# Performance work log

Measured on AMD Instinct MI355X. Metric: run time of the kernel, lower is better.

## Reference

```python
import jax, jax.numpy as jnp
import numpy as np

B, S, D, C, K, V = 128, 512, 300, 300, 3, 30000  # batch, seq, embed=hidden, capsule, categories, vocab
PAD_INDEX = 0
SQUASH_EPS = 1e-8
MASK_NEG = -1e9


def squash(x, axis=-1):
    # v * (|v|^2 / (1+|v|^2)) / |v|
    sq = jnp.sum(x * x, axis=axis, keepdims=True)
    return (sq / (1.0 + sq)) * x / jnp.sqrt(sq + SQUASH_EPS)


def setup_inputs() -> dict:
    key = jax.random.key(0)
    ks = jax.random.split(key, 11)
    return {
        "sentence": jax.random.randint(ks[0], (B, S), 0, V),
        "aspect": jax.random.randint(ks[1], (B,), 0, V),
        "category_alpha": jax.random.uniform(ks[2], (B, S), dtype=jnp.float32),
        "embed": jax.random.normal(ks[3], (V, D), dtype=jnp.float32) * 0.02,
        "W_s": jax.random.normal(ks[4], (D, C), dtype=jnp.float32) * 0.02,
        "b_s": jnp.zeros((C,), dtype=jnp.float32),
        "W_a": jax.random.normal(ks[5], (D, C), dtype=jnp.float32) * 0.02,
        "b_a": jnp.zeros((C,), dtype=jnp.float32),
        "W_att": jax.random.normal(ks[6], (C, C), dtype=jnp.float32) * 0.02,
        "guide_capsule": jax.random.normal(ks[7], (K, C), dtype=jnp.float32) * 0.02,
        "guide_weight": jax.random.normal(ks[8], (C, C), dtype=jnp.float32) * 0.02,
        "scale": jnp.asarray(5.0, dtype=jnp.float32),
    }


def reference(sentence, aspect, category_alpha, embed, W_s, b_s, W_a, b_a,
              W_att, guide_capsule, guide_weight, scale):
    mask = sentence != PAD_INDEX                      # [B,S]
    emb = embed[sentence]                             # [B,S,D]
    asp = embed[aspect]                               # [B,D]

    # element_wise_mul (vectorized): per-token alpha weighting
    caml = emb * category_alpha[..., None]            # [B,S,D]
    cavl = jnp.sum(caml, axis=1)                      # [B,D] (unused in non-Cav path)
    del cavl

    # _sentence_encode stand-in (abstract in source): alpha-weighted embeddings
    sent_enc = caml                                   # [B,S,hidden=D]

    primary = squash(sent_enc @ W_s + b_s)            # [B,S,C]
    aspect_capsule = squash(asp @ W_a + b_a)          # [B,C]

    # bilinear attention weights with padding mask, softmax over sequence
    scores = jnp.einsum('bsc,cd,bd->bs', primary, W_att, aspect_capsule)
    scores = jnp.where(mask, scores, MASK_NEG)
    norm_weight = jax.nn.softmax(scores, axis=-1)     # [B,S]

    # capsule-guided routing
    guide = squash(guide_capsule)                     # [K,C]
    gm = jnp.einsum('bsc,cd,kd->bsk', primary, guide_weight, guide)
    gm = jax.nn.softmax(gm, axis=-1) * norm_weight[..., None] * scale
    category_capsule = squash(jnp.einsum('bsk,bsc->bkc', gm, primary))  # [B,K,C]

    return jnp.sqrt(jnp.sum(category_capsule * category_capsule, axis=-1))  # [B,K]
```

## Files before the change

kernel.cpp:

```cpp
#include <hip/hip_runtime.h>

#define NV 30000
#define NB 128
#define NS 512
#define ND 300
#define NC 300
#define CP 304
#define KPAD 320
#define MASK_NEG -1e9f
#define SQ_EPS 1e-8f

typedef __attribute__((ext_vector_type(4))) float f32x4;
typedef __attribute__((ext_vector_type(8))) __bf16 bf16x8;

__device__ __forceinline__ unsigned short f2bf(float x){
  unsigned int u = __float_as_uint(x);
  u += 0x7FFFu + ((u >> 16) & 1u);
  return (unsigned short)(u >> 16);
}
__device__ __forceinline__ float bf2f(unsigned short h){
  return __uint_as_float(((unsigned int)h) << 16);
}

__global__ __launch_bounds__(320) void k0_prep(
    const float* __restrict__ Ws, const float* __restrict__ Watt,
    const float* __restrict__ Gw, const float* __restrict__ bs,
    const float* __restrict__ gcap,
    unsigned short* __restrict__ wt, float* __restrict__ att_t,
    float* __restrict__ gwt, float* __restrict__ bsp, float* __restrict__ gpad)
{
  int bid = blockIdx.x, tid = threadIdx.x;
  __shared__ float red[320];
  if (bid < 80) {
    #pragma unroll
    for (int r = 0; r < 4; r++){
      int id = bid*1280 + r*320 + tid;
      int n = id / 320, k = id - n*320;
      float v = (n < NC && k < ND) ? Ws[k*NC + n] : 0.f;
      wt[n*KPAD + k] = f2bf(v);
    }
  } else if (bid < 151) {
    #pragma unroll
    for (int r = 0; r < 4; r++){
      int id = (bid-80)*1280 + r*320 + tid;
      if (id < ND*NC){ int c = id / ND, d = id - c*ND; att_t[d*CP + c] = Watt[id]; }
    }
  } else if (bid < 222) {
    #pragma unroll
    for (int r = 0; r < 4; r++){
      int id = (bid-151)*1280 + r*320 + tid;
      if (id < ND*NC){ int c = id / ND, d = id - c*ND; gwt[d*CP + c] = Gw[id]; }
    }
  } else if (bid == 222) {
    if (tid < CP) bsp[tid] = (tid < NC) ? bs[tid] : 0.f;
  } else {
    int k = bid - 223;
    float g = (tid < NC) ? gcap[k*NC + tid] : 0.f;
    red[tid] = g*g; __syncthreads();
    if (tid < 64){
      float s = red[tid]+red[tid+64]+red[tid+128]+red[tid+192]+red[tid+256];
      #pragma unroll
      for (int off = 32; off > 0; off >>= 1) s += __shfl_xor(s, off);
      if (tid == 0) red[0] = s;
    }
    __syncthreads();
    float sq = red[0];
    float ss = (sq/(1.f+sq))/sqrtf(sq + SQ_EPS);
    if (tid < CP) gpad[k*CP + tid] = g*ss;
  }
}

#define ANB 4
__global__ __launch_bounds__(320) void k2_aspect(
    const int* __restrict__ aspect, const float* __restrict__ embed,
    const float* __restrict__ Wa, const float* __restrict__ ba,
    const float* __restrict__ att_t, const float* __restrict__ gwt,
    const float* __restrict__ gpad,
    float* __restrict__ tbuf, float* __restrict__ gbuf)
{
  int bid = blockIdx.x, tid = threadIdx.x;
  __shared__ float red[320];
  if (bid < NB/ANB) {
    __shared__ float vec[ANB][CP];
    int b0 = bid*ANB;
    for (int i = tid; i < ANB*CP; i += 320){
      int bi = i / CP, c = i - bi*CP;
      int a = aspect[b0 + bi];
      vec[bi][c] = (c < ND) ? embed[(size_t)a*ND + c] : 0.f;
    }
    __syncthreads();
    float z[ANB] = {0.f,0.f,0.f,0.f};
    if (tid < NC){
      #pragma unroll
      for (int i = 0; i < ANB; i++) z[i] = ba[tid];
      for (int d = 0; d < ND; d++){
        float wv = Wa[d*NC + tid];
        #pragma unroll
        for (int i = 0; i < ANB; i++) z[i] += vec[i][d]*wv;
      }
    }
    float ssv[ANB];
    for (int i = 0; i < ANB; i++){
      red[tid] = (tid < NC) ? z[i]*z[i] : 0.f;
      __syncthreads();
      if (tid < 64){
        float s = red[tid]+red[tid+64]+red[tid+128]+red[tid+192]+red[tid+256];
        #pragma unroll
        for (int off = 32; off > 0; off >>= 1) s += __shfl_xor(s, off);
        if (tid == 0) red[0] = s;
      }
      __syncthreads();
      float sq = red[0];
      ssv[i] = (sq/(1.f+sq))/sqrtf(sq + SQ_EPS);
      __syncthreads();
    }
    if (tid < CP){
      #pragma unroll
      for (int i = 0; i < ANB; i++) vec[i][tid] = (tid < NC) ? z[i]*ssv[i] : 0.f;
    }
    __syncthreads();
    float t[ANB] = {0.f,0.f,0.f,0.f};
    if (tid < NC){
      for (int d = 0; d < ND; d++){
        float av = att_t[d*CP + tid];
        #pragma unroll
        for (int i = 0; i < ANB; i++) t[i] += av*vec[i][d];
      }
    }
    if (tid < CP){
      #pragma unroll
      for (int i = 0; i < ANB; i++) tbuf[(b0+i)*CP + tid] = (tid < NC) ? t[i] : 0.f;
    }
  } else {
    int k = bid - NB/ANB;
    float t = 0.f;
    if (tid < NC){
      for (int d = 0; d < ND; d++) t += gwt[d*CP + tid]*gpad[k*CP + d];
    }
    if (tid < CP) gbuf[k*CP + tid] = (tid < NC) ? t : 0.f;
  }
}

#define BM 128
#define BKT 64
#define LDK 72
__global__ __launch_bounds__(512) void k1_gemm(
    const float* __restrict__ embed, const unsigned short* __restrict__ wt,
    unsigned short* __restrict__ E)
{
  __shared__ unsigned short lds_a[BM*LDK];
  __shared__ unsigned short lds_b[320*LDK];
  int tid = threadIdx.x;
  int lane = tid & 63, wid = tid >> 6;
  int wrow = wid >> 2, wcol = wid & 3;
  int rowbase = blockIdx.x * BM;
  f32x4 acc[4][5];
  f32x4 zero = {0.f,0.f,0.f,0.f};
  #pragma unroll
  for (int m = 0; m < 4; m++)
    #pragma unroll
    for (int n = 0; n < 5; n++) acc[m][n] = zero;

  for (int k0 = 0; k0 < KPAD; k0 += BKT){
    #pragma unroll
    for (int r = 0; r < 4; r++){
      int id = r*512 + tid;
      int row = id >> 4, k4 = (id & 15) << 2;
      int gk = k0 + k4, grow = rowbase + row;
      float4 v = {0.f,0.f,0.f,0.f};
      if (grow < NV && gk < ND) v = *(const float4*)(embed + (size_t)grow*ND + gk);
      unsigned int lo = (unsigned int)f2bf(v.x) | ((unsigned int)f2bf(v.y) << 16);
      unsigned int hi = (unsigned int)f2bf(v.z) | ((unsigned int)f2bf(v.w) << 16);
      uint2 pk; pk.x = lo; pk.y = hi;
      *(uint2*)(lds_a + row*LDK + k4) = pk;
    }
    #pragma unroll
    for (int r = 0; r < 5; r++){
      int id = r*512 + tid;
      int n = id >> 3, koff = (id & 7) << 3;
      uint4 v = *(const uint4*)(wt + n*KPAD + k0 + koff);
      *(uint4*)(lds_b + n*LDK + koff) = v;
    }
    __syncthreads();
    #pragma unroll
    for (int kk = 0; kk < BKT; kk += 32){
      bf16x8 af[4], bfr[5];
      int kidx = kk + (lane >> 4)*8;
      int arow = wrow*64 + (lane & 15);
      int brow = wcol*80 + (lane & 15);
      #pragma unroll
      for (int m = 0; m < 4; m++) af[m] = *(const bf16x8*)(lds_a + (arow + m*16)*LDK + kidx);
      #pragma unroll
      for (int n = 0; n < 5; n++) bfr[n] = *(const bf16x8*)(lds_b + (brow + n*16)*LDK + kidx);
      #pragma unroll
      for (int m = 0; m < 4; m++)
        #pragma unroll
        for (int n = 0; n < 5; n++)
          acc[m][n] = __builtin_amdgcn_mfma_f32_16x16x32_bf16(af[m], bfr[n], acc[m][n], 0, 0, 0);
    }
    __syncthreads();
  }
  int colb = wcol*80 + (lane & 15);
  int rowb = rowbase + wrow*64 + ((lane >> 4) << 2);
  #pragma unroll
  for (int m = 0; m < 4; m++)
    #pragma unroll
    for (int n = 0; n < 5; n++)
      #pragma unroll
      for (int j = 0; j < 4; j++){
        int row = rowb + m*16 + j;
        int col = colb + n*16;
        if (row < NV && col < CP) E[(size_t)row*CP + col] = f2bf(acc[m][n][j]);
      }
}

__global__ __launch_bounds__(256) void k3_token(
    const int* __restrict__ sentence, const float* __restrict__ alphaA,
    const unsigned short* __restrict__ E, const float* __restrict__ tbuf,
    const float* __restrict__ gbuf, const float* __restrict__ bsp,
    float* __restrict__ scoreB, float* __restrict__ ssB, float* __restrict__ uuB)
{
  int tid = threadIdx.x;
  int lane = tid & 63;
  int wg = (blockIdx.x << 2) + (tid >> 6);
  int tok = sentence[wg];
  float al = alphaA[wg];
  int b = wg >> 9;
  const unsigned short* erow = E + (size_t)tok*CP;
  const float* trow = tbuf + b*CP;
  float sq = 0.f, sc = 0.f, u0 = 0.f, u1 = 0.f, u2 = 0.f;
  auto body = [&](int c){
    uint2 e2 = *(const uint2*)(erow + c);
    float4 tv = *(const float4*)(trow + c);
    float4 g0 = *(const float4*)(gbuf + c);
    float4 g1 = *(const float4*)(gbuf + CP + c);
    float4 g2 = *(const float4*)(gbuf + 2*CP + c);
    float4 bv = *(const float4*)(bsp + c);
    float y0 = al*bf2f((unsigned short)(e2.x & 0xffffu)) + bv.x;
    float y1 = al*bf2f((unsigned short)(e2.x >> 16)) + bv.y;
    float y2 = al*bf2f((unsigned short)(e2.y & 0xffffu)) + bv.z;
    float y3 = al*bf2f((unsigned short)(e2.y >> 16)) + bv.w;
    sq += y0*y0 + y1*y1 + y2*y2 + y3*y3;
    sc += y0*tv.x + y1*tv.y + y2*tv.z + y3*tv.w;
    u0 += y0*g0.x + y1*g0.y + y2*g0.z + y3*g0.w;
    u1 += y0*g1.x + y1*g1.y + y2*g1.z + y3*g1.w;
    u2 += y0*g2.x + y1*g2.y + y2*g2.z + y3*g2.w;
  };
  body(lane << 2);
  if (lane < 12) body(256 + (lane << 2));
  #pragma unroll
  for (int off = 32; off > 0; off >>= 1){
    sq += __shfl_xor(sq, off);
    sc += __shfl_xor(sc, off);
    u0 += __shfl_xor(u0, off);
    u1 += __shfl_xor(u1, off);
    u2 += __shfl_xor(u2, off);
  }
  if (lane == 0){
    float ssv = (sq/(1.f+sq))/sqrtf(sq + SQ_EPS);
    scoreB[wg] = (tok != 0) ? ssv*sc : MASK_NEG;
    ssB[wg] = ssv;
    uuB[wg*3+0] = ssv*u0;
    uuB[wg*3+1] = ssv*u1;
    uuB[wg*3+2] = ssv*u2;
  }
}

__global__ __launch_bounds__(512) void k4_softmax(
    const float* __restrict__ scoreB, const float* __restrict__ uuB,
    const float* __restrict__ ssB, const float* __restrict__ alphaA,
    const float* __restrict__ scale_p,
    float* __restrict__ coef, float* __restrict__ sb)
{
  int b = blockIdx.x, tid = threadIdx.x;
  int idx = (b << 9) + tid;
  __shared__ float red[512];
  float scv = scoreB[idx];
  red[tid] = scv; __syncthreads();
  if (tid < 64){
    float s = red[tid];
    #pragma unroll
    for (int o = 64; o < 512; o += 64) s = fmaxf(s, red[tid+o]);
    #pragma unroll
    for (int off = 32; off > 0; off >>= 1) s = fmaxf(s, __shfl_xor(s, off));
    if (tid == 0) red[0] = s;
  }
  __syncthreads();
  float m = red[0];
  __syncthreads();
  float e = expf(scv - m);
  red[tid] = e; __syncthreads();
  if (tid < 64){
    float s = 0.f;
    #pragma unroll
    for (int o = 0; o < 512; o += 64) s += red[tid+o];
    #pragma unroll
    for (int off = 32; off > 0; off >>= 1) s += __shfl_xor(s, off);
    if (tid == 0) red[0] = s;
  }
  __syncthreads();
  float Z = red[0];
  __syncthreads();
  float nw = e / Z;
  float v0 = uuB[idx*3+0], v1 = uuB[idx*3+1], v2 = uuB[idx*3+2];
  float mk = fmaxf(v0, fmaxf(v1, v2));
  float e0 = expf(v0-mk), e1 = expf(v1-mk), e2 = expf(v2-mk);
  float wf = nw * scale_p[0] / (e0+e1+e2);
  float w0 = e0*wf, w1 = e1*wf, w2 = e2*wf;
  float ssv = ssB[idx];
  float ca = ssv * alphaA[idx];
  coef[idx*3+0] = w0*ca; coef[idx*3+1] = w1*ca; coef[idx*3+2] = w2*ca;
  float s0 = w0*ssv, s1 = w1*ssv, s2 = w2*ssv;
  red[tid] = s0; __syncthreads();
  if (tid < 64){
    float s = 0.f;
    #pragma unroll
    for (int o = 0; o < 512; o += 64) s += red[tid+o];
    #pragma unroll
    for (int off = 32; off > 0; off >>= 1) s += __shfl_xor(s, off);
    if (tid == 0) sb[b*3+0] = s;
  }
  __syncthreads();
  red[tid] = s1; __syncthreads();
  if (tid < 64){
    float s = 0.f;
    #pragma unroll
    for (int o = 0; o < 512; o += 64) s += red[tid+o];
    #pragma unroll
    for (int off = 32; off > 0; off >>= 1) s += __shfl_xor(s, off);
    if (tid == 0) sb[b*3+1] = s;
  }
  __syncthreads();
  red[tid] = s2; __syncthreads();
  if (tid < 64){
    float s = 0.f;
    #pragma unroll
    for (int o = 0; o < 512; o += 64) s += red[tid+o];
    #pragma unroll
    for (int off = 32; off > 0; off >>= 1) s += __shfl_xor(s, off);
    if (tid == 0) sb[b*3+2] = s;
  }
}

__global__ __launch_bounds__(320) void k5_accum(
    const int* __restrict__ sentence, const unsigned short* __restrict__ E,
    const float* __restrict__ coef, float* __restrict__ part)
{
  int bid = blockIdx.x;
  int tid = threadIdx.x;
  int tbase = bid << 7;
  __shared__ int toks[128];
  __shared__ float cfs[384];
  if (tid < 128) toks[tid] = sentence[tbase + tid];
  cfs[tid] = coef[tbase*3 + tid];
  if (tid < 64) cfs[320+tid] = coef[tbase*3 + 320 + tid];
  __syncthreads();
  if (tid < CP){
    float a0 = 0.f, a1 = 0.f, a2 = 0.f;
    for (int i = 0; i < 128; i++){
      float ev = bf2f(E[(size_t)toks[i]*CP + tid]);
      a0 += cfs[i*3+0]*ev;
      a1 += cfs[i*3+1]*ev;
      a2 += cfs[i*3+2]*ev;
    }
    float* p = part + (size_t)bid*3*CP;
    p[tid] = a0; p[CP+tid] = a1; p[2*CP+tid] = a2;
  }
}

__global__ __launch_bounds__(320) void k6_norm(
    const float* __restrict__ part, const float* __restrict__ sb,
    const float* __restrict__ bsp, float* __restrict__ out)
{
  int bid = blockIdx.x;
  int b = bid / 3, k = bid - b*3;
  int tid = threadIdx.x;
  __shared__ float red[320];
  float v = 0.f;
  if (tid < CP){
    v = sb[bid]*bsp[tid];
    #pragma unroll
    for (int ch = 0; ch < 4; ch++)
      v += part[((size_t)(b*4+ch)*3 + k)*CP + tid];
  }
  red[tid] = v*v; __syncthreads();
  if (tid < 64){
    float s = red[tid]+red[tid+64]+red[tid+128]+red[tid+192]+red[tid+256];
    #pragma unroll
    for (int off = 32; off > 0; off >>= 1) s += __shfl_xor(s, off);
    if (tid == 0){
      float sq = s;
      out[bid] = (sq/(1.f+sq))*sqrtf(sq)/sqrtf(sq + SQ_EPS);
    }
  }
}

extern "C" void kernel_launch(void* const* d_in, const int* in_sizes, int n_in,
                              void* d_out, int out_size, void* d_ws, size_t ws_size,
                              hipStream_t stream)
{
  (void)in_sizes; (void)n_in; (void)out_size; (void)ws_size;
  const int*   sentence = (const int*)d_in[0];
  const int*   aspect   = (const int*)d_in[1];
  const float* alpha    = (const float*)d_in[2];
  const float* embed    = (const float*)d_in[3];
  const float* Ws       = (const float*)d_in[4];
  const float* bs       = (const float*)d_in[5];
  const float* Wa       = (const float*)d_in[6];
  const float* ba       = (const float*)d_in[7];
  const float* Watt     = (const float*)d_in[8];
  const float* gcap     = (const float*)d_in[9];
  const float* gw       = (const float*)d_in[10];
  const float* scale    = (const float*)d_in[11];
  float* out = (float*)d_out;

  char* w = (char*)d_ws;
  auto alloc = [&](size_t bytes)->char*{
    char* p = w; w += (bytes + 255) & ~(size_t)255; return p;
  };
  unsigned short* WT  = (unsigned short*)alloc((size_t)KPAD*KPAD*2);
  unsigned short* E   = (unsigned short*)alloc((size_t)NV*CP*2);
  float* ATT = (float*)alloc((size_t)ND*CP*4);
  float* GWT = (float*)alloc((size_t)ND*CP*4);
  float* BSP = (float*)alloc(CP*4);
  float* GPD = (float*)alloc(3*CP*4);
  float* TBF = (float*)alloc((size_t)NB*CP*4);
  float* GBF = (float*)alloc(3*CP*4);
  float* SCO = (float*)alloc((size_t)NB*NS*4);
  float* SSB = (float*)alloc((size_t)NB*NS*4);
  float* UUB = (float*)alloc((size_t)NB*NS*3*4);
  float* COF = (float*)alloc((size_t)NB*NS*3*4);
  float* SBB = (float*)alloc(NB*3*4);
  float* PRT = (float*)alloc((size_t)NB*4*3*CP*4);

  k0_prep<<<226, 320, 0, stream>>>(Ws, Watt, gw, bs, gcap, WT, ATT, GWT, BSP, GPD);
  k2_aspect<<<NB/ANB + 3, 320, 0, stream>>>(aspect, embed, Wa, ba, ATT, GWT, GPD, TBF, GBF);
  k1_gemm<<<(NV + BM - 1)/BM, 512, 0, stream>>>(embed, WT, E);
  k3_token<<<NB*NS/4, 256, 0, stream>>>(sentence, alpha, E, TBF, GBF, BSP, SCO, SSB, UUB);
  k4_softmax<<<NB, 512, 0, stream>>>(SCO, UUB, SSB, alpha, scale, COF, SBB);
  k5_accum<<<NB*4, 320, 0, stream>>>(sentence, E, COF, PRT);
  k6_norm<<<NB*3, 320, 0, stream>>>(PRT, SBB, BSP, out);
}
```

Measured before the change: 112.4 us.

## Merge prep and aspect kernels, halve GEMM tile, fuse norm into accumulate

Folds the weight-transpose prep and the aspect/guide projection kernels into one launch. W_att and guide_weight are now read row-wise with wave reductions, so their transposed copies are no longer built. The W_s transpose goes through an LDS tile. The E-projection GEMM row tile drops from 128 to 64 to launch more blocks. k3 processes four tokens per wave with a quarter of the blocks. The final norm kernel is merged into k5_accum through an atomic last-block counter, which k4 resets. These changes cut launch count and redundant transposes, but add atomic and fence overhead and may lower GEMM reuse per block.

Measured after the change: 200.5 us. +78.3%, slower.

```diff
diff --git a/kernel.cpp b/kernel.cpp
--- a/kernel.cpp
+++ b/kernel.cpp
@@ -6,7 +6,7 @@
 #define ND 300
 #define NC 300
 #define CP 304
-#define KPAD 320
+#define KP 320
 #define MASK_NEG -1e9f
 #define SQ_EPS 1e-8f
 
@@ -22,126 +22,170 @@
   return __uint_as_float(((unsigned int)h) << 16);
 }
 
-__global__ __launch_bounds__(320) void k0_prep(
+__device__ __forceinline__ float block_sum320(float v, float* red, int tid){
+  red[tid] = v; __syncthreads();
+  float s = 0.f;
+  if (tid < 64){
+    s = red[tid]+red[tid+64]+red[tid+128]+red[tid+192]+red[tid+256];
+    #pragma unroll
+    for (int off = 32; off > 0; off >>= 1) s += __shfl_xor(s, off);
+    if (tid == 0) red[0] = s;
+  }
+  __syncthreads();
+  s = red[0];
+  __syncthreads();
+  return s;
+}
+
+__global__ __launch_bounds__(320) void kprep(
     const float* __restrict__ Ws, const float* __restrict__ Watt,
     const float* __restrict__ Gw, const float* __restrict__ bs,
-    const float* __restrict__ gcap,
-    unsigned short* __restrict__ wt, float* __restrict__ att_t,
-    float* __restrict__ gwt, float* __restrict__ bsp, float* __restrict__ gpad)
+    const float* __restrict__ gcap, const int* __restrict__ aspect,
+    const float* __restrict__ embed, const float* __restrict__ Wa,
+    const float* __restrict__ ba,
+    unsigned short* __restrict__ wt, float* __restrict__ bsp,
+    float* __restrict__ tbuf, float* __restrict__ gbuf)
 {
   int bid = blockIdx.x, tid = threadIdx.x;
+  int lane = tid & 63, wid = tid >> 6;
   __shared__ float red[320];
-  if (bid < 80) {
-    #pragma unroll
-    for (int r = 0; r < 4; r++){
-      int id = bid*1280 + r*320 + tid;
-      int n = id / 320, k = id - n*320;
-      float v = (n < NC && k < ND) ? Ws[k*NC + n] : 0.f;
-      wt[n*KPAD + k] = f2bf(v);
-    }
-  } else if (bid < 151) {
-    #pragma unroll
-    for (int r = 0; r < 4; r++){
-      int id = (bid-80)*1280 + r*320 + tid;
-      if (id < ND*NC){ int c = id / ND, d = id - c*ND; att_t[d*CP + c] = Watt[id]; }
-    }
-  } else if (bid < 222) {
-    #pragma unroll
-    for (int r = 0; r < 4; r++){
-      int id = (bid-151)*1280 + r*320 + tid;
-      if (id < ND*NC){ int c = id / ND, d = id - c*ND; gwt[d*CP + c] = Gw[id]; }
-    }
-  } else if (bid == 222) {
+  if (bid < 25) {
+    __shared__ float t[64][65];
+    int kt = bid / 5, nt = bid - kt*5;
+    #pragma unroll
+    for (int i = 0; i < 13; i++){
+      int idx = i*320 + tid;
+      if (idx < 4096){
+        int r = idx >> 6, c = idx & 63;
+        int gk = kt*64 + r, gn = nt*64 + c;
+        t[r][c] = (gk < ND && gn < NC) ? Ws[gk*NC + gn] : 0.f;
+      }
+    }
+    __syncthreads();
+    #pragma unroll
+    for (int i = 0; i < 13; i++){
+      int idx = i*320 + tid;
+      if (idx < 4096){
+        int n = idx >> 6, k = idx & 63;
+        wt[(nt*64 + n)*KP + kt*64 + k] = f2bf(t[k][n]);
+      }
+    }
+  } else if (bid == 25) {
     if (tid < CP) bsp[tid] = (tid < NC) ? bs[tid] : 0.f;
-  } else {
-    int k = bid - 223;
-    float g = (tid < NC) ? gcap[k*NC + tid] : 0.f;
-    red[tid] = g*g; __syncthreads();
-    if (tid < 64){
-      float s = red[tid]+red[tid+64]+red[tid+128]+red[tid+192]+red[tid+256];
-      #pragma unroll
-      for (int off = 32; off > 0; off >>= 1) s += __shfl_xor(s, off);
-      if (tid == 0) red[0] = s;
-    }
-    __syncthreads();
-    float sq = red[0];
-    float ss = (sq/(1.f+sq))/sqrtf(sq + SQ_EPS);
-    if (tid < CP) gpad[k*CP + tid] = g*ss;
-  }
-}
-
-#define ANB 4
-__global__ __launch_bounds__(320) void k2_aspect(
-    const int* __restrict__ aspect, const float* __restrict__ embed,
-    const float* __restrict__ Wa, const float* __restrict__ ba,
-    const float* __restrict__ att_t, const float* __restrict__ gwt,
-    const float* __restrict__ gpad,
-    float* __restrict__ tbuf, float* __restrict__ gbuf)
-{
-  int bid = blockIdx.x, tid = threadIdx.x;
-  __shared__ float red[320];
-  if (bid < NB/ANB) {
-    __shared__ float vec[ANB][CP];
-    int b0 = bid*ANB;
-    for (int i = tid; i < ANB*CP; i += 320){
+  } else if (bid < 58) {
+    __shared__ float vec[4][CP];
+    int b0 = (bid - 26) * 4;
+    for (int i = tid; i < 4*CP; i += 320){
       int bi = i / CP, c = i - bi*CP;
       int a = aspect[b0 + bi];
       vec[bi][c] = (c < ND) ? embed[(size_t)a*ND + c] : 0.f;
     }
     __syncthreads();
-    float z[ANB] = {0.f,0.f,0.f,0.f};
+    float z[4] = {0.f,0.f,0.f,0.f};
     if (tid < NC){
       #pragma unroll
-      for (int i = 0; i < ANB; i++) z[i] = ba[tid];
+      for (int i = 0; i < 4; i++) z[i] = ba[tid];
       for (int d = 0; d < ND; d++){
         float wv = Wa[d*NC + tid];
         #pragma unroll
-        for (int i = 0; i < ANB; i++) z[i] += vec[i][d]*wv;
-      }
-    }
-    float ssv[ANB];
-    for (int i = 0; i < ANB; i++){
-      red[tid] = (tid < NC) ? z[i]*z[i] : 0.f;
-      __syncthreads();
-      if (tid < 64){
-        float s = red[tid]+red[tid+64]+red[tid+128]+red[tid+192]+red[tid+256];
-        #pragma unroll
-        for (int off = 32; off > 0; off >>= 1) s += __shfl_xor(s, off);
-        if (tid == 0) red[0] = s;
-      }
-      __syncthreads();
-      float sq = red[0];
+        for (int i = 0; i < 4; i++) z[i] += vec[i][d]*wv;
+      }
+    }
+    float ssv[4];
+    #pragma unroll
+    for (int i = 0; i < 4; i++){
+      float sq = block_sum320((tid < NC) ? z[i]*z[i] : 0.f, red, tid);
       ssv[i] = (sq/(1.f+sq))/sqrtf(sq + SQ_EPS);
-      __syncthreads();
     }
     if (tid < CP){
       #pragma unroll
-      for (int i = 0; i < ANB; i++) vec[i][tid] = (tid < NC) ? z[i]*ssv[i] : 0.f;
-    }
-    __syncthreads();
-    float t[ANB] = {0.f,0.f,0.f,0.f};
-    if (tid < NC){
-      for (int d = 0; d < ND; d++){
-        float av = att_t[d*CP + tid];
-        #pragma unroll
-        for (int i = 0; i < ANB; i++) t[i] += av*vec[i][d];
-      }
+      for (int i = 0; i < 4; i++) vec[i][tid] = (tid < NC) ? z[i]*ssv[i] : 0.f;
+    }
+    __syncthreads();
+    float capr[4][5];
+    #pragma unroll
+    for (int j = 0; j < 5; j++){
+      int d = j*64 + lane;
+      #pragma unroll
+      for (int i = 0; i < 4; i++) capr[i][j] = (d < CP) ? vec[i][d] : 0.f;
+    }
+    for (int c = wid; c < NC; c += 5){
+      const float* wr = Watt + (size_t)c*NC;
+      float a0=0.f,a1=0.f,a2=0.f,a3=0.f;
+      #pragma unroll
+      for (int j = 0; j < 5; j++){
+        int d = j*64 + lane;
+        float w = (d < ND) ? wr[d] : 0.f;
+        a0 += w*capr[0][j]; a1 += w*capr[1][j];
+        a2 += w*capr[2][j]; a3 += w*capr[3][j];
+      }
+      #pragma unroll
+      for (int off = 32; off > 0; off >>= 1){
+        a0 += __shfl_xor(a0, off); a1 += __shfl_xor(a1, off);
+        a2 += __shfl_xor(a2, off); a3 += __shfl_xor(a3, off);
+      }
+      if (lane == 0){
+        tbuf[(b0+0)*CP + c] = a0; tbuf[(b0+1)*CP + c] = a1;
+        tbuf[(b0+2)*CP + c] = a2; tbuf[(b0+3)*CP + c] = a3;
+      }
+    }
+    if (tid < 16){
+      int bi = tid >> 2, cc = NC + (tid & 3);
+      tbuf[(b0+bi)*CP + cc] = 0.f;
+    }
+  } else {
+    __shared__ float gv[3][CP];
+    int gb = bid - 58, c0 = gb*100;
+    for (int i = tid; i < 3*CP; i += 320){
+      int k = i / CP, c = i - k*CP;
+      gv[k][c] = (c < NC) ? gcap[k*NC + c] : 0.f;
+    }
+    __syncthreads();
+    float ssk[3];
+    #pragma unroll
+    for (int k = 0; k < 3; k++){
+      float g = (tid < CP) ? gv[k][tid] : 0.f;
+      float sq = block_sum320(g*g, red, tid);
+      ssk[k] = (sq/(1.f+sq))/sqrtf(sq + SQ_EPS);
     }
     if (tid < CP){
       #pragma unroll
-      for (int i = 0; i < ANB; i++) tbuf[(b0+i)*CP + tid] = (tid < NC) ? t[i] : 0.f;
-    }
-  } else {
-    int k = bid - NB/ANB;
-    float t = 0.f;
-    if (tid < NC){
-      for (int d = 0; d < ND; d++) t += gwt[d*CP + tid]*gpad[k*CP + d];
-    }
-    if (tid < CP) gbuf[k*CP + tid] = (tid < NC) ? t : 0.f;
-  }
-}
-
-#define BM 128
+      for (int k = 0; k < 3; k++) gv[k][tid] *= ssk[k];
+    }
+    __syncthreads();
+    float gr[3][5];
+    #pragma unroll
+    for (int j = 0; j < 5; j++){
+      int d = j*64 + lane;
+      #pragma unroll
+      for (int k = 0; k < 3; k++) gr[k][j] = (d < CP) ? gv[k][d] : 0.f;
+    }
+    int cend = c0 + 100;
+    for (int c = c0 + wid; c < cend; c += 5){
+      const float* wr = Gw + (size_t)c*NC;
+      float a0=0.f,a1=0.f,a2=0.f;
+      #pragma unroll
+      for (int j = 0; j < 5; j++){
+        int d = j*64 + lane;
+        float w = (d < ND) ? wr[d] : 0.f;
+        a0 += w*gr[0][j]; a1 += w*gr[1][j]; a2 += w*gr[2][j];
+      }
+      #pragma unroll
+      for (int off = 32; off > 0; off >>= 1){
+        a0 += __shfl_xor(a0, off); a1 += __shfl_xor(a1, off); a2 += __shfl_xor(a2, off);
+      }
+      if (lane == 0){
+        gbuf[0*CP + c] = a0; gbuf[1*CP + c] = a1; gbuf[2*CP + c] = a2;
+      }
+    }
+    if (gb == 0 && tid < 12){
+      int k = tid >> 2, cc = NC + (tid & 3);
+      gbuf[k*CP + cc] = 0.f;
+    }
+  }
+}
+
+#define BM 64
 #define BKT 64
 #define LDK 72
 __global__ __launch_bounds__(512) void k1_gemm(
@@ -149,21 +193,21 @@
     unsigned short* __restrict__ E)
 {
   __shared__ unsigned short lds_a[BM*LDK];
-  __shared__ unsigned short lds_b[320*LDK];
+  __shared__ unsigned short lds_b[KP*LDK];
   int tid = threadIdx.x;
   int lane = tid & 63, wid = tid >> 6;
   int wrow = wid >> 2, wcol = wid & 3;
   int rowbase = blockIdx.x * BM;
-  f32x4 acc[4][5];
+  f32x4 acc[2][5];
   f32x4 zero = {0.f,0.f,0.f,0.f};
   #pragma unroll
-  for (int m = 0; m < 4; m++)
+  for (int m = 0; m < 2; m++)
     #pragma unroll
     for (int n = 0; n < 5; n++) acc[m][n] = zero;
 
-  for (int k0 = 0; k0 < KPAD; k0 += BKT){
-    #pragma unroll
-    for (int r = 0; r < 4; r++){
+  for (int k0 = 0; k0 < KP; k0 += BKT){
+    #pragma unroll
+    for (int r = 0; r < 2; r++){
       int id = r*512 + tid;
       int row = id >> 4, k4 = (id & 15) << 2;
       int gk = k0 + k4, grow = rowbase + row;
@@ -178,22 +222,22 @@
     for (int r = 0; r < 5; r++){
       int id = r*512 + tid;
       int n = id >> 3, koff = (id & 7) << 3;
-      uint4 v = *(const uint4*)(wt + n*KPAD + k0 + koff);
+      uint4 v = *(const uint4*)(wt + n*KP + k0 + koff);
       *(uint4*)(lds_b + n*LDK + koff) = v;
     }
     __syncthreads();
     #pragma unroll
     for (int kk = 0; kk < BKT; kk += 32){
-      bf16x8 af[4], bfr[5];
+      bf16x8 af[2], bfr[5];
       int kidx = kk + (lane >> 4)*8;
-      int arow = wrow*64 + (lane & 15);
+      int arow = wrow*32 + (lane & 15);
       int brow = wcol*80 + (lane & 15);
       #pragma unroll
-      for (int m = 0; m < 4; m++) af[m] = *(const bf16x8*)(lds_a + (arow + m*16)*LDK + kidx);
+      for (int m = 0; m < 2; m++) af[m] = *(const bf16x8*)(lds_a + (arow + m*16)*LDK + kidx);
       #pragma unroll
       for (int n = 0; n < 5; n++) bfr[n] = *(const bf16x8*)(lds_b + (brow + n*16)*LDK + kidx);
       #pragma unroll
-      for (int m = 0; m < 4; m++)
+      for (int m = 0; m < 2; m++)
         #pragma unroll
         for (int n = 0; n < 5; n++)
           acc[m][n] = __builtin_amdgcn_mfma_f32_16x16x32_bf16(af[m], bfr[n], acc[m][n], 0, 0, 0);
@@ -201,9 +245,9 @@
     __syncthreads();
   }
   int colb = wcol*80 + (lane & 15);
-  int rowb = rowbase + wrow*64 + ((lane >> 4) << 2);
+  int rowb = rowbase + wrow*32 + ((lane >> 4) << 2);
   #pragma unroll
-  for (int m = 0; m < 4; m++)
+  for (int m = 0; m < 2; m++)
     #pragma unroll
     for (int n = 0; n < 5; n++)
       #pragma unroll
@@ -222,47 +266,51 @@
 {
   int tid = threadIdx.x;
   int lane = tid & 63;
-  int wg = (blockIdx.x << 2) + (tid >> 6);
-  int tok = sentence[wg];
-  float al = alphaA[wg];
-  int b = wg >> 9;
-  const unsigned short* erow = E + (size_t)tok*CP;
-  const float* trow = tbuf + b*CP;
-  float sq = 0.f, sc = 0.f, u0 = 0.f, u1 = 0.f, u2 = 0.f;
-  auto body = [&](int c){
-    uint2 e2 = *(const uint2*)(erow + c);
-    float4 tv = *(const float4*)(trow + c);
-    float4 g0 = *(const float4*)(gbuf + c);
-    float4 g1 = *(const float4*)(gbuf + CP + c);
-    float4 g2 = *(const float4*)(gbuf + 2*CP + c);
-    float4 bv = *(const float4*)(bsp + c);
-    float y0 = al*bf2f((unsigned short)(e2.x & 0xffffu)) + bv.x;
-    float y1 = al*bf2f((unsigned short)(e2.x >> 16)) + bv.y;
-    float y2 = al*bf2f((unsigned short)(e2.y & 0xffffu)) + bv.z;
-    float y3 = al*bf2f((unsigned short)(e2.y >> 16)) + bv.w;
-    sq += y0*y0 + y1*y1 + y2*y2 + y3*y3;
-    sc += y0*tv.x + y1*tv.y + y2*tv.z + y3*tv.w;
-    u0 += y0*g0.x + y1*g0.y + y2*g0.z + y3*g0.w;
-    u1 += y0*g1.x + y1*g1.y + y2*g1.z + y3*g1.w;
-    u2 += y0*g2.x + y1*g2.y + y2*g2.z + y3*g2.w;
-  };
-  body(lane << 2);
-  if (lane < 12) body(256 + (lane << 2));
+  int gw0 = (blockIdx.x << 2) + (tid >> 6);
   #pragma unroll
-  for (int off = 32; off > 0; off >>= 1){
-    sq += __shfl_xor(sq, off);
-    sc += __shfl_xor(sc, off);
-    u0 += __shfl_xor(u0, off);
-    u1 += __shfl_xor(u1, off);
-    u2 += __shfl_xor(u2, off);
-  }
-  if (lane == 0){
-    float ssv = (sq/(1.f+sq))/sqrtf(sq + SQ_EPS);
-    scoreB[wg] = (tok != 0) ? ssv*sc : MASK_NEG;
-    ssB[wg] = ssv;
-    uuB[wg*3+0] = ssv*u0;
-    uuB[wg*3+1] = ssv*u1;
-    uuB[wg*3+2] = ssv*u2;
+  for (int it = 0; it < 4; it++){
+    int wg = gw0 + (it << 14);
+    int tok = sentence[wg];
+    float al = alphaA[wg];
+    int b = wg >> 9;
+    const unsigned short* erow = E + (size_t)tok*CP;
+    const float* trow = tbuf + b*CP;
+    float sq = 0.f, sc = 0.f, u0 = 0.f, u1 = 0.f, u2 = 0.f;
+    auto body = [&](int c){
+      uint2 e2 = *(const uint2*)(erow + c);
+      float4 tv = *(const float4*)(trow + c);
+      float4 g0 = *(const float4*)(gbuf + c);
+      float4 g1 = *(const float4*)(gbuf + CP + c);
+      float4 g2 = *(const float4*)(gbuf + 2*CP + c);
+      float4 bv = *(const float4*)(bsp + c);
+      float y0 = al*bf2f((unsigned short)(e2.x & 0xffffu)) + bv.x;
+      float y1 = al*bf2f((unsigned short)(e2.x >> 16)) + bv.y;
+      float y2 = al*bf2f((unsigned short)(e2.y & 0xffffu)) + bv.z;
+      float y3 = al*bf2f((unsigned short)(e2.y >> 16)) + bv.w;
+      sq += y0*y0 + y1*y1 + y2*y2 + y3*y3;
+      sc += y0*tv.x + y1*tv.y + y2*tv.z + y3*tv.w;
+      u0 += y0*g0.x + y1*g0.y + y2*g0.z + y3*g0.w;
+      u1 += y0*g1.x + y1*g1.y + y2*g1.z + y3*g1.w;
+      u2 += y0*g2.x + y1*g2.y + y2*g2.z + y3*g2.w;
+    };
+    body(lane << 2);
+    if (lane < 12) body(256 + (lane << 2));
+    #pragma unroll
+    for (int off = 32; off > 0; off >>= 1){
+      sq += __shfl_xor(sq, off);
+      sc += __shfl_xor(sc, off);
+      u0 += __shfl_xor(u0, off);
+      u1 += __shfl_xor(u1, off);
+      u2 += __shfl_xor(u2, off);
+    }
+    if (lane == 0){
+      float ssv = (sq/(1.f+sq))/sqrtf(sq + SQ_EPS);
+      scoreB[wg] = (tok != 0) ? ssv*sc : MASK_NEG;
+      ssB[wg] = ssv;
+      uuB[wg*3+0] = ssv*u0;
+      uuB[wg*3+1] = ssv*u1;
+      uuB[wg*3+2] = ssv*u2;
+    }
   }
 }
 
@@ -270,11 +318,12 @@
     const float* __restrict__ scoreB, const float* __restrict__ uuB,
     const float* __restrict__ ssB, const float* __restrict__ alphaA,
     const float* __restrict__ scale_p,
-    float* __restrict__ coef, float* __restrict__ sb)
+    float* __restrict__ coef, float* __restrict__ sb, int* __restrict__ CNT)
 {
   int b = blockIdx.x, tid = threadIdx.x;
   int idx = (b << 9) + tid;
   __shared__ float red[512];
+  if (tid == 0) CNT[b] = 0;
   float scv = scoreB[idx];
   red[tid] = scv; __syncthreads();
   if (tid < 64){
@@ -344,13 +393,18 @@
 
 __global__ __launch_bounds__(320) void k5_accum(
     const int* __restrict__ sentence, const unsigned short* __restrict__ E,
-    const float* __restrict__ coef, float* __restrict__ part)
+    const float* __restrict__ coef, float* __restrict__ part,
+    int* __restrict__ CNT, const float* __restrict__ sb,
+    const float* __restrict__ bsp, float* __restrict__ out)
 {
   int bid = blockIdx.x;
   int tid = threadIdx.x;
+  int b = bid >> 2;
   int tbase = bid << 7;
   __shared__ int toks[128];
   __shared__ float cfs[384];
+  __shared__ float red[320];
+  __shared__ int sflag;
   if (tid < 128) toks[tid] = sentence[tbase + tid];
   cfs[tid] = coef[tbase*3 + tid];
   if (tid < 64) cfs[320+tid] = coef[tbase*3 + 320 + tid];
@@ -366,31 +420,32 @@
     float* p = part + (size_t)bid*3*CP;
     p[tid] = a0; p[CP+tid] = a1; p[2*CP+tid] = a2;
   }
-}
-
-__global__ __launch_bounds__(320) void k6_norm(
-    const float* __restrict__ part, const float* __restrict__ sb,
-    const float* __restrict__ bsp, float* __restrict__ out)
-{
-  int bid = blockIdx.x;
-  int b = bid / 3, k = bid - b*3;
-  int tid = threadIdx.x;
-  __shared__ float red[320];
-  float v = 0.f;
-  if (tid < CP){
-    v = sb[bid]*bsp[tid];
-    #pragma unroll
-    for (int ch = 0; ch < 4; ch++)
-      v += part[((size_t)(b*4+ch)*3 + k)*CP + tid];
-  }
-  red[tid] = v*v; __syncthreads();
-  if (tid < 64){
-    float s = red[tid]+red[tid+64]+red[tid+128]+red[tid+192]+red[tid+256];
-    #pragma unroll
-    for (int off = 32; off > 0; off >>= 1) s += __shfl_xor(s, off);
-    if (tid == 0){
-      float sq = s;
-      out[bid] = (sq/(1.f+sq))*sqrtf(sq)/sqrtf(sq + SQ_EPS);
+  __threadfence();
+  __syncthreads();
+  if (tid == 0) sflag = atomicAdd(&CNT[b], 1);
+  __syncthreads();
+  if (sflag == 3){
+    __threadfence();
+    #pragma unroll
+    for (int k = 0; k < 3; k++){
+      float v = 0.f;
+      if (tid < CP){
+        v = sb[b*3+k]*bsp[tid];
+        #pragma unroll
+        for (int ch = 0; ch < 4; ch++)
+          v += part[((size_t)(b*4+ch)*3 + k)*CP + tid];
+      }
+      red[tid] = v*v; __syncthreads();
+      if (tid < 64){
+        float s = red[tid]+red[tid+64]+red[tid+128]+red[tid+192]+red[tid+256];
+        #pragma unroll
+        for (int off = 32; off > 0; off >>= 1) s += __shfl_xor(s, off);
+        if (tid == 0){
+          float sq = s;
+          out[b*3+k] = (sq/(1.f+sq))*sqrtf(sq)/sqrtf(sq + SQ_EPS);
+        }
+      }
+      __syncthreads();
     }
   }
 }
@@ -418,12 +473,9 @@
   auto alloc = [&](size_t bytes)->char*{
     char* p = w; w += (bytes + 255) & ~(size_t)255; return p;
   };
-  unsigned short* WT  = (unsigned short*)alloc((size_t)KPAD*KPAD*2);
+  unsigned short* WT  = (unsigned short*)alloc((size_t)KP*KP*2);
   unsigned short* E   = (unsigned short*)alloc((size_t)NV*CP*2);
-  float* ATT = (float*)alloc((size_t)ND*CP*4);
-  float* GWT = (float*)alloc((size_t)ND*CP*4);
   float* BSP = (float*)alloc(CP*4);
-  float* GPD = (float*)alloc(3*CP*4);
   float* TBF = (float*)alloc((size_t)NB*CP*4);
   float* GBF = (float*)alloc(3*CP*4);
   float* SCO = (float*)alloc((size_t)NB*NS*4);
@@ -432,12 +484,12 @@
   float* COF = (float*)alloc((size_t)NB*NS*3*4);
   float* SBB = (float*)alloc(NB*3*4);
   float* PRT = (float*)alloc((size_t)NB*4*3*CP*4);
-
-  k0_prep<<<226, 320, 0, stream>>>(Ws, Watt, gw, bs, gcap, WT, ATT, GWT, BSP, GPD);
-  k2_aspect<<<NB/ANB + 3, 320, 0, stream>>>(aspect, embed, Wa, ba, ATT, GWT, GPD, TBF, GBF);
+  int*   CNT = (int*)alloc(NB*4);
+
+  kprep<<<61, 320, 0, stream>>>(Ws, Watt, gw, bs, gcap, aspect, embed, Wa, ba,
+                                WT, BSP, TBF, GBF);
   k1_gemm<<<(NV + BM - 1)/BM, 512, 0, stream>>>(embed, WT, E);
-  k3_token<<<NB*NS/4, 256, 0, stream>>>(sentence, alpha, E, TBF, GBF, BSP, SCO, SSB, UUB);
-  k4_softmax<<<NB, 512, 0, stream>>>(SCO, UUB, SSB, alpha, scale, COF, SBB);
-  k5_accum<<<NB*4, 320, 0, stream>>>(sentence, E, COF, PRT);
-  k6_norm<<<NB*3, 320, 0, stream>>>(PRT, SBB, BSP, out);
-}
+  k3_token<<<4096, 256, 0, stream>>>(sentence, alpha, E, TBF, GBF, BSP, SCO, SSB, UUB);
+  k4_softmax<<<NB, 512, 0, stream>>>(SCO, UUB, SSB, alpha, scale, COF, SBB, CNT);
+  k5_accum<<<NB*4, 320, 0, stream>>>(sentence, E, COF, PRT, CNT, SBB, BSP, out);
+}
```
